# Kernel optimization log

Measured on AMD Instinct MI355X. Metric: run time of the kernel, lower is better.

The kernel has to match this reference:

```python
import jax, jax.numpy as jnp
import numpy as np

D_MODEL = 1024
NUM_TILES = 8
BATCH = 4096
TEMPERATURE = 0.5

gelu = lambda x: jax.nn.gelu(x, approximate=False)  # torch nn.GELU default = exact erf


def setup_inputs() -> dict:
    key = jax.random.key(0)
    ks = jax.random.split(key, 12)
    d, t = D_MODEL, NUM_TILES
    s = lambda fan_in: 1.0 / np.sqrt(fan_in)
    return {
        "x": jax.random.normal(ks[0], (BATCH, d), jnp.float32),
        # router: Linear(d,d) -> GELU -> Linear(d,num_tiles); weights stored (in,out)
        "Wr1": jax.random.uniform(ks[1], (d, d), jnp.float32, -s(d), s(d)),
        "br1": jax.random.uniform(ks[2], (d,), jnp.float32, -s(d), s(d)),
        "Wr2": jax.random.uniform(ks[3], (d, t), jnp.float32, -s(d), s(d)),
        "br2": jax.random.uniform(ks[4], (t,), jnp.float32, -s(d), s(d)),
        # tile nets: Linear(d,2d) -> GELU -> Linear(2d,d), stacked over tiles
        "W1": jax.random.uniform(ks[5], (t, d, 2 * d), jnp.float32, -s(d), s(d)),
        "b1": jax.random.uniform(ks[6], (t, 2 * d), jnp.float32, -s(d), s(d)),
        "W2": jax.random.uniform(ks[7], (t, 2 * d, d), jnp.float32, -s(2 * d), s(2 * d)),
        "b2": jax.random.uniform(ks[8], (t, d), jnp.float32, -s(2 * d), s(2 * d)),
        # output projection Linear(d,d)
        "Wo": jax.random.uniform(ks[9], (d, d), jnp.float32, -s(d), s(d)),
        "bo": jax.random.uniform(ks[10], (d,), jnp.float32, -s(d), s(d)),
    }


def reference(x, Wr1, br1, Wr2, br2, W1, b1, W2, b2, Wo, bo):
    # router logits / temperature
    route_logits = (gelu(x @ Wr1 + br1) @ Wr2 + br2) / TEMPERATURE  # (B, T)
    tile_idx = jnp.argmax(route_logits, axis=-1)                    # (B,)

    # hard routing: compute all tile MLPs, then select the argmax tile per token
    # (dense equivalent of per-sample dispatch; same math as the torch loop)
    h = gelu(jnp.einsum("bd,tdf->btf", x, W1) + b1[None])           # (B, T, 2d)
    tile_out = jnp.einsum("btf,tfd->btd", h, W2) + b2[None]         # (B, T, d)
    selected = jnp.take_along_axis(tile_out, tile_idx[:, None, None], axis=1)[:, 0]  # (B, d)

    output = selected @ Wo + bo                                     # (B, d)
    return output, tile_idx, route_logits
```

## Files before the change

### kernel.cpp

```cpp
#include <hip/hip_runtime.h>
#include <hip/hip_bf16.h>
#include <math.h>
#include <stdint.h>

typedef __bf16 bf16_t;
typedef __bf16 bf16x4 __attribute__((ext_vector_type(4)));
typedef __bf16 bf16x8 __attribute__((ext_vector_type(8)));
typedef float  f32x4  __attribute__((ext_vector_type(4)));

#define BATCH   4096
#define DM      1024
#define DFF     2048
#define NTILES  8
#define MAXXB   40

__device__ __forceinline__ float gelu_exact(float x) {
    return 0.5f * x * (1.0f + erff(x * 0.70710678118654752440f));
}

__device__ __forceinline__ void async_ld16(const bf16_t* g, bf16_t* l) {
    __builtin_amdgcn_global_load_lds(
        (const __attribute__((address_space(1))) void*)g,
        (__attribute__((address_space(3))) void*)l, 16, 0, 0);
}

__device__ __forceinline__ f32x4 mfma16(bf16x8 a, bf16x8 b, f32x4 c) {
    return __builtin_amdgcn_mfma_f32_16x16x32_bf16(a, b, c, 0, 0, 0);
}

template<bool LO>
__device__ void tconv64_body(const float* __restrict__ src, bf16_t* __restrict__ outh,
                             bf16_t* __restrict__ outl, int K, int N, int kt, int nt,
                             float4* t ) {
    const int tid = threadIdx.x;
    const int k0 = kt * 64, n0 = nt * 64;
#pragma unroll
    for (int p = 0; p < 4; ++p) {
        int row = p * 16 + (tid >> 4);
        int c = tid & 15;
        float4 v = *(const float4*)(src + (size_t)(k0 + row) * N + n0 + c * 4);
        t[row * 16 + (c ^ ((row >> 2) & 15))] = v;
    }
    __syncthreads();
    const int n = tid >> 2, b = tid & 3;
    const float* tf = (const float*)t;
    float v[16];
#pragma unroll
    for (int i = 0; i < 16; ++i) {
        int k = 16 * b + i;
        int f4 = k * 16 + ((n >> 2) ^ ((k >> 2) & 15));
        v[i] = tf[f4 * 4 + (n & 3)];
    }
    bf16x8 h0, h1;
#pragma unroll
    for (int i = 0; i < 8; ++i) { h0[i] = (bf16_t)v[i]; h1[i] = (bf16_t)v[8 + i]; }
    size_t oi = (size_t)(n0 + n) * K + k0 + 16 * b;
    *(bf16x8*)(outh + oi) = h0;
    *(bf16x8*)(outh + oi + 8) = h1;
    if constexpr (LO) {
        bf16x8 l0, l1;
#pragma unroll
        for (int i = 0; i < 8; ++i) {
            l0[i] = (bf16_t)(v[i] - (float)h0[i]);
            l1[i] = (bf16_t)(v[8 + i] - (float)h1[i]);
        }
        *(bf16x8*)(outl + oi) = l0;
        *(bf16x8*)(outl + oi + 8) = l1;
    }
}

#define NCVT2 2048
#define NSQ64 256
#define NW1   4096
#define NW2   4096
#define PREP_GRID (NCVT2 + NSQ64 + NSQ64 + NW1 + NW2)

__global__ __launch_bounds__(256) void prep_kernel(
    const float* __restrict__ x, const float* __restrict__ Wr1, const float* __restrict__ Wo,
    const float* __restrict__ W1, const float* __restrict__ W2,
    bf16_t* __restrict__ xh, bf16_t* __restrict__ xl,
    bf16_t* __restrict__ Wr1h, bf16_t* __restrict__ Wr1l, bf16_t* __restrict__ Wot,
    bf16_t* __restrict__ W1t, bf16_t* __restrict__ W2t) {
    __shared__ float4 t[64 * 16];
    int b = blockIdx.x;
    if (b < NCVT2) {
        size_t i = (size_t)b * 256 + threadIdx.x;
        const float4* x4 = (const float4*)x;
        float4 v0 = x4[2 * i], v1 = x4[2 * i + 1];
        float f[8] = {v0.x, v0.y, v0.z, v0.w, v1.x, v1.y, v1.z, v1.w};
        bf16x8 h, l;
#pragma unroll
        for (int j = 0; j < 8; ++j) { h[j] = (bf16_t)f[j]; l[j] = (bf16_t)(f[j] - (float)h[j]); }
        *(bf16x8*)(xh + i * 8) = h;
        *(bf16x8*)(xl + i * 8) = l;
        return;
    }
    b -= NCVT2;
    if (b < NSQ64) { tconv64_body<true >(Wr1, Wr1h, Wr1l, DM, DM, b >> 4, b & 15, t); return; }
    b -= NSQ64;
    if (b < NSQ64) { tconv64_body<false>(Wo, Wot, nullptr, DM, DM, b >> 4, b & 15, t); return; }
    b -= NSQ64;
    if (b < NW1) {
        int mat = b >> 9, r = b & 511;
        size_t off = (size_t)mat * DM * DFF;
        tconv64_body<false>(W1 + off, W1t + off, nullptr, DM, DFF, r >> 5, r & 31, t);
        return;
    }
    b -= NW1;
    {
        int mat = b >> 9, r = b & 511;
        size_t off = (size_t)mat * DM * DFF;
        tconv64_body<false>(W2 + off, W2t + off, nullptr, DFF, DM, r >> 4, r & 15, t);
    }
}

template<bool SPLIT, bool GATHER, bool GELU, bool SCATTER, bool OUTF32>
__global__ __launch_bounds__(512) void gemm_kernel(
    const bf16_t* __restrict__ A, const bf16_t* __restrict__ Alo,
    const bf16_t* __restrict__ Bt, const bf16_t* __restrict__ Btlo,
    const float* __restrict__ bias,
    float* __restrict__ outF, bf16_t* __restrict__ outB,
    const int* __restrict__ perm, const int* __restrict__ counts,
    int M, int N, int K) {
    int tile = 0, rb, cnt = M;
    const int* permT = nullptr;
    if constexpr (GATHER) {
        int xb = blockIdx.x, t = 0, c = 0;
        while (t < NTILES) {
            c = counts[t];
            int nbk = (c + 127) >> 7;
            if (xb < nbk) break;
            xb -= nbk; ++t;
        }
        if (t == NTILES) return;
        tile = t;
        rb = xb * 128;
        cnt = c;
        permT = perm + tile * BATCH;
    } else {
        rb = blockIdx.x * 128;
    }
    Bt   += (size_t)tile * K * N;
    if constexpr (SPLIT) Btlo += (size_t)tile * K * N;
    bias += (size_t)tile * N;

    constexpr int BUF = 128 * 32;
    __shared__ __align__(16) bf16_t As[2 * BUF];
    __shared__ __align__(16) bf16_t Bs[2 * BUF];
    __shared__ __align__(16) bf16_t Asl[SPLIT ? 2 * BUF : 8];
    __shared__ __align__(16) bf16_t Bsl[SPLIT ? 2 * BUF : 8];

    const int lane = threadIdx.x & 63;
    const int wave = threadIdx.x >> 6;
    const int wm = wave & 1, wn = wave >> 1;
    const int nb = blockIdx.y * 128;

    const int srow = lane >> 2;
    const int scol = ((lane & 3) ^ (srow & 3)) * 8;
    const int row = wave * 16 + srow;
    int arow;
    if constexpr (GATHER) {
        int pos = rb + row;
        if (pos > cnt - 1) pos = cnt - 1;
        arow = permT[pos];
    } else {
        arow = rb + row;
    }
    const size_t aoff = (size_t)arow * K + scol;
    const size_t boff = (size_t)(nb + row) * K + scol;

    f32x4 acc[4][2];
#pragma unroll
    for (int i = 0; i < 4; ++i)
#pragma unroll
        for (int j = 0; j < 2; ++j) acc[i][j] = (f32x4){0.f, 0.f, 0.f, 0.f};

    const int lr = lane & 15, lq = lane >> 4;
    const int rdoff = (lr * 4 + (lq ^ (lr & 3))) * 8;

    auto stage = [&](int k0, int buf) {
        async_ld16(A  + aoff + k0, &As[buf * BUF + wave * 512]);
        async_ld16(Bt + boff + k0, &Bs[buf * BUF + wave * 512]);
        if constexpr (SPLIT) {
            async_ld16(Alo  + aoff + k0, &Asl[buf * BUF + wave * 512]);
            async_ld16(Btlo + boff + k0, &Bsl[buf * BUF + wave * 512]);
        }
    };

    auto compute = [&](int cur) {
        bf16x8 af[4], bfr[2], afl[4], bfl[2];
#pragma unroll
        for (int i = 0; i < 4; ++i) {
            af[i] = *(const bf16x8*)&As[cur * BUF + (wm * 4 + i) * 512 + rdoff];
            if constexpr (SPLIT)
                afl[i] = *(const bf16x8*)&Asl[cur * BUF + (wm * 4 + i) * 512 + rdoff];
        }
#pragma unroll
        for (int j = 0; j < 2; ++j) {
            bfr[j] = *(const bf16x8*)&Bs[cur * BUF + (wn * 2 + j) * 512 + rdoff];
            if constexpr (SPLIT)
                bfl[j] = *(const bf16x8*)&Bsl[cur * BUF + (wn * 2 + j) * 512 + rdoff];
        }
#pragma unroll
        for (int i = 0; i < 4; ++i)
#pragma unroll
            for (int j = 0; j < 2; ++j) {
                acc[i][j] = mfma16(af[i], bfr[j], acc[i][j]);
                if constexpr (SPLIT) {
                    acc[i][j] = mfma16(af[i], bfl[j], acc[i][j]);
                    acc[i][j] = mfma16(afl[i], bfr[j], acc[i][j]);
                }
            }
    };

    stage(0, 0);
    int cur = 0;
    for (int k0 = 0; k0 < K; k0 += 32, cur ^= 1) {
        __syncthreads();
        if (k0 + 32 < K) stage(k0 + 32, cur ^ 1);
        compute(cur);
    }

#pragma unroll
    for (int i = 0; i < 4; ++i) {
#pragma unroll
        for (int j = 0; j < 2; ++j) {
#pragma unroll
            for (int r = 0; r < 4; ++r) {
                int m = wm * 64 + i * 16 + lq * 4 + r;
                int n = wn * 32 + j * 16 + lr;
                int pos = rb + m;
                if constexpr (GATHER) { if (pos >= cnt) continue; }
                int grow;
                if constexpr (SCATTER) grow = permT[pos];
                else                   grow = pos;
                int gn = nb + n;
                float v = acc[i][j][r] + bias[gn];
                if constexpr (GELU) v = gelu_exact(v);
                if constexpr (OUTF32) outF[(size_t)grow * N + gn] = v;
                else                  outB[(size_t)grow * N + gn] = (bf16_t)v;
            }
        }
    }
}

__global__ __launch_bounds__(256) void router2_kernel(
    const float* __restrict__ Hr, const float* __restrict__ Wr2, const float* __restrict__ br2,
    float* __restrict__ outLog, float* __restrict__ outIdx,
    int* __restrict__ counts, int* __restrict__ perm) {
    __shared__ float w2s[DM * 9];
    __shared__ int h[NTILES], base[NTILES];
    const int tid = threadIdx.x;
    if (tid < NTILES) h[tid] = 0;
    for (int e = tid; e < DM * 8; e += 256) {
        int k = e >> 3, j = e & 7;
        w2s[k * 9 + j] = Wr2[e];
    }
    __syncthreads();

    const int lane = tid & 63, wave = tid >> 6;
    const int sub = lane >> 4;
    const int lr16 = lane & 15;
    const int row = blockIdx.x * 16 + wave * 4 + sub;

    const float4* Hr4 = (const float4*)Hr;
    float acc[8];
#pragma unroll
    for (int j = 0; j < 8; ++j) acc[j] = 0.f;

#pragma unroll
    for (int i = 0; i < 16; ++i) {
        int f = lr16 + i * 16;
        float4 hv = Hr4[(size_t)row * 256 + f];
        float hx[4] = {hv.x, hv.y, hv.z, hv.w};
        int kbase = f * 4;
#pragma unroll
        for (int d = 0; d < 4; ++d) {
            float xv = hx[d];
            const float* w = &w2s[(kbase + d) * 9];
#pragma unroll
            for (int j = 0; j < 8; ++j) acc[j] += xv * w[j];
        }
    }
#pragma unroll
    for (int off = 8; off; off >>= 1)
#pragma unroll
        for (int j = 0; j < 8; ++j) acc[j] += __shfl_down(acc[j], off);

    int bi = 0, rank = 0;
    if (lr16 == 0) {
        float best = -1e30f;
        float lg[8];
#pragma unroll
        for (int j = 0; j < 8; ++j) {
            float v = (acc[j] + br2[j]) * 2.0f;
            lg[j] = v;
            if (v > best) { best = v; bi = j; }
        }
        float4 lo = {lg[0], lg[1], lg[2], lg[3]};
        float4 hi = {lg[4], lg[5], lg[6], lg[7]};
        *(float4*)(outLog + (size_t)row * 8)     = lo;
        *(float4*)(outLog + (size_t)row * 8 + 4) = hi;
        outIdx[row] = (float)bi;
        rank = atomicAdd(&h[bi], 1);
    }
    __syncthreads();
    if (tid < NTILES && h[tid] > 0) base[tid] = atomicAdd(&counts[tid], h[tid]);
    __syncthreads();
    if (lr16 == 0) perm[bi * BATCH + base[bi] + rank] = row;
}

extern "C" void kernel_launch(void* const* d_in, const int* in_sizes, int n_in,
                              void* d_out, int out_size, void* d_ws, size_t ws_size,
                              hipStream_t stream) {
    const float* x   = (const float*)d_in[0];
    const float* Wr1 = (const float*)d_in[1];
    const float* br1 = (const float*)d_in[2];
    const float* Wr2 = (const float*)d_in[3];
    const float* br2 = (const float*)d_in[4];
    const float* W1  = (const float*)d_in[5];
    const float* b1  = (const float*)d_in[6];
    const float* W2  = (const float*)d_in[7];
    const float* b2  = (const float*)d_in[8];
    const float* Wo  = (const float*)d_in[9];
    const float* bo  = (const float*)d_in[10];

    char* ws = (char*)d_ws;
    size_t o = 0;
    auto carve = [&](size_t bytes) { char* p = ws + o; o = (o + bytes + 255) & ~(size_t)255; return p; };
    bf16_t* Wr1h = (bf16_t*)carve((size_t)DM * DM * 2);
    bf16_t* Wr1l = (bf16_t*)carve((size_t)DM * DM * 2);
    bf16_t* Wot  = (bf16_t*)carve((size_t)DM * DM * 2);
    bf16_t* W1t  = (bf16_t*)carve((size_t)NTILES * DM * DFF * 2);
    bf16_t* W2t  = (bf16_t*)carve((size_t)NTILES * DM * DFF * 2);
    bf16_t* xh   = (bf16_t*)carve((size_t)BATCH * DM * 2);
    bf16_t* xl   = (bf16_t*)carve((size_t)BATCH * DM * 2);
    bf16_t* H1   = (bf16_t*)carve((size_t)BATCH * DFF * 2);
    bf16_t* sel  = (bf16_t*)carve((size_t)BATCH * DM * 2);
    float*  Hr   = (float*)carve((size_t)BATCH * DM * 4);
    int*    counts = (int*)carve(NTILES * sizeof(int));
    int*    perm   = (int*)carve((size_t)NTILES * BATCH * sizeof(int));

    float* outMain = (float*)d_out;
    float* outIdx  = outMain + (size_t)BATCH * DM;
    float* outLog  = outIdx + BATCH;

    hipMemsetAsync(counts, 0, NTILES * sizeof(int), stream);

    prep_kernel<<<PREP_GRID, 256, 0, stream>>>(x, Wr1, Wo, W1, W2,
                                               xh, xl, Wr1h, Wr1l, Wot, W1t, W2t);

    gemm_kernel<true, false, true, false, true><<<dim3(BATCH / 128, DM / 128, 1), 512, 0, stream>>>(
        xh, xl, Wr1h, Wr1l, br1, Hr, nullptr, nullptr, nullptr, BATCH, DM, DM);

    router2_kernel<<<BATCH / 16, 256, 0, stream>>>(Hr, Wr2, br2, outLog, outIdx, counts, perm);

    gemm_kernel<false, true, true, true, false><<<dim3(MAXXB, DFF / 128, 1), 512, 0, stream>>>(
        xh, nullptr, W1t, nullptr, b1, nullptr, H1, perm, counts, BATCH, DFF, DM);

    gemm_kernel<false, true, false, true, false><<<dim3(MAXXB, DM / 128, 1), 512, 0, stream>>>(
        H1, nullptr, W2t, nullptr, b2, nullptr, sel, perm, counts, BATCH, DM, DFF);

    gemm_kernel<false, false, false, false, true><<<dim3(BATCH / 128, DM / 128, 1), 512, 0, stream>>>(
        sel, nullptr, Wot, nullptr, bo, outMain, nullptr, nullptr, nullptr, BATCH, DM, DM);
}
```

Measured before the change: 365.4 us.

## Triple-buffer GEMM LDS pipeline and stream low-precision split operands through registers

Replaces the two-stage LDS double buffer, which synchronised every K step, with a three-stage ring. Explicit vmcnt waits and raw barriers let each tile prefetch two steps ahead. For the split-precision path, the low-part A and B fragments are now loaded straight from global memory into registers one step ahead instead of being staged through LDS. MFMA sections are raised in wave priority with s_setprio. This aims to hide global-load latency and cut LDS traffic and footprint. The risk is that the hand-set vmcnt counts are wrong, and the direct low-part loads ignore the gather permutation on the A rows.

```diff
diff --git a/kernel.cpp b/kernel.cpp
--- a/kernel.cpp
+++ b/kernel.cpp
@@ -145,10 +145,8 @@
     bias += (size_t)tile * N;
 
     constexpr int BUF = 128 * 32;
-    __shared__ __align__(16) bf16_t As[2 * BUF];
-    __shared__ __align__(16) bf16_t Bs[2 * BUF];
-    __shared__ __align__(16) bf16_t Asl[SPLIT ? 2 * BUF : 8];
-    __shared__ __align__(16) bf16_t Bsl[SPLIT ? 2 * BUF : 8];
+    __shared__ __align__(16) bf16_t As[3 * BUF];
+    __shared__ __align__(16) bf16_t Bs[3 * BUF];
 
     const int lane = threadIdx.x & 63;
     const int wave = threadIdx.x >> 6;
@@ -178,47 +176,80 @@
     const int lr = lane & 15, lq = lane >> 4;
     const int rdoff = (lr * 4 + (lq ^ (lr & 3))) * 8;
 
+    size_t aloOff[4], bloOff[2];
+    if constexpr (SPLIT) {
+#pragma unroll
+        for (int i = 0; i < 4; ++i)
+            aloOff[i] = (size_t)(rb + (wm * 4 + i) * 16 + lr) * K + lq * 8;
+#pragma unroll
+        for (int j = 0; j < 2; ++j)
+            bloOff[j] = (size_t)(nb + (wn * 2 + j) * 16 + lr) * K + lq * 8;
+    }
+
     auto stage = [&](int k0, int buf) {
         async_ld16(A  + aoff + k0, &As[buf * BUF + wave * 512]);
         async_ld16(Bt + boff + k0, &Bs[buf * BUF + wave * 512]);
+    };
+
+    auto loadLo = [&](int k0, bf16x8* a, bf16x8* b) {
+#pragma unroll
+        for (int i = 0; i < 4; ++i) a[i] = *(const bf16x8*)(Alo  + aloOff[i] + k0);
+#pragma unroll
+        for (int j = 0; j < 2; ++j) b[j] = *(const bf16x8*)(Btlo + bloOff[j] + k0);
+    };
+
+    auto compute = [&](int cur, const bf16x8* afl, const bf16x8* bfl) {
+        bf16x8 af[4], bfr[2];
+#pragma unroll
+        for (int i = 0; i < 4; ++i)
+            af[i] = *(const bf16x8*)&As[cur * BUF + (wm * 4 + i) * 512 + rdoff];
+#pragma unroll
+        for (int j = 0; j < 2; ++j)
+            bfr[j] = *(const bf16x8*)&Bs[cur * BUF + (wn * 2 + j) * 512 + rdoff];
+        __builtin_amdgcn_s_setprio(1);
+#pragma unroll
+        for (int i = 0; i < 4; ++i)
+#pragma unroll
+            for (int j = 0; j < 2; ++j)
+                acc[i][j] = mfma16(af[i], bfr[j], acc[i][j]);
         if constexpr (SPLIT) {
-            async_ld16(Alo  + aoff + k0, &Asl[buf * BUF + wave * 512]);
-            async_ld16(Btlo + boff + k0, &Bsl[buf * BUF + wave * 512]);
-        }
-    };
-
-    auto compute = [&](int cur) {
-        bf16x8 af[4], bfr[2], afl[4], bfl[2];
-#pragma unroll
-        for (int i = 0; i < 4; ++i) {
-            af[i] = *(const bf16x8*)&As[cur * BUF + (wm * 4 + i) * 512 + rdoff];
-            if constexpr (SPLIT)
-                afl[i] = *(const bf16x8*)&Asl[cur * BUF + (wm * 4 + i) * 512 + rdoff];
-        }
-#pragma unroll
-        for (int j = 0; j < 2; ++j) {
-            bfr[j] = *(const bf16x8*)&Bs[cur * BUF + (wn * 2 + j) * 512 + rdoff];
-            if constexpr (SPLIT)
-                bfl[j] = *(const bf16x8*)&Bsl[cur * BUF + (wn * 2 + j) * 512 + rdoff];
-        }
-#pragma unroll
-        for (int i = 0; i < 4; ++i)
-#pragma unroll
-            for (int j = 0; j < 2; ++j) {
-                acc[i][j] = mfma16(af[i], bfr[j], acc[i][j]);
-                if constexpr (SPLIT) {
+#pragma unroll
+            for (int i = 0; i < 4; ++i)
+#pragma unroll
+                for (int j = 0; j < 2; ++j) {
                     acc[i][j] = mfma16(af[i], bfl[j], acc[i][j]);
                     acc[i][j] = mfma16(afl[i], bfr[j], acc[i][j]);
                 }
-            }
+        }
+        __builtin_amdgcn_s_setprio(0);
     };
 
+    bf16x8 aflC[4], bflC[2], aflN[4], bflN[2];
     stage(0, 0);
-    int cur = 0;
-    for (int k0 = 0; k0 < K; k0 += 32, cur ^= 1) {
-        __syncthreads();
-        if (k0 + 32 < K) stage(k0 + 32, cur ^ 1);
-        compute(cur);
+    stage(32, 1);
+    if constexpr (SPLIT) loadLo(0, aflN, bflN);
+
+    int bufc = 0;
+    for (int k0 = 0; k0 < K; k0 += 32) {
+        if (k0 + 32 < K) {
+            if constexpr (SPLIT) asm volatile("s_waitcnt vmcnt(8)" ::: "memory");
+            else                 asm volatile("s_waitcnt vmcnt(2)" ::: "memory");
+        } else {
+            asm volatile("s_waitcnt vmcnt(0)" ::: "memory");
+        }
+        __builtin_amdgcn_s_barrier();
+        int nb3 = bufc + 2; if (nb3 >= 3) nb3 -= 3;
+        if (k0 + 64 < K) stage(k0 + 64, nb3);
+        if constexpr (SPLIT) {
+#pragma unroll
+            for (int i = 0; i < 4; ++i) aflC[i] = aflN[i];
+#pragma unroll
+            for (int j = 0; j < 2; ++j) bflC[j] = bflN[j];
+            if (k0 + 32 < K) loadLo(k0 + 32, aflN, bflN);
+        }
+        __builtin_amdgcn_sched_barrier(0);
+        compute(bufc, aflC, bflC);
+        if (++bufc == 3) bufc = 0;
     }
 
 #pragma unroll
```

After: 399.2 us. +9.3%, slower.

## Pipeline weight transpose-convert with async LDS loads over four-tile slabs

Applied to the files above, without the earlier changes.

The prep kernel's transpose-and-convert of weights now has each block process a slab of four 64x64 tiles instead of one. It uses global_load_lds async copies into a double-buffered shared tile, so the next tile's load overlaps the current tile's transpose and bf16 store. This cuts the block count and the load latency exposed per tile. In exchange it doubles LDS per block, adds manual waitcnt/barrier sequencing, and leaves fewer blocks to spread across CUs.

```diff
diff --git a/kernel.cpp b/kernel.cpp
--- a/kernel.cpp
+++ b/kernel.cpp
@@ -29,51 +29,79 @@
 }
 
 template<bool LO>
-__device__ void tconv64_body(const float* __restrict__ src, bf16_t* __restrict__ outh,
-                             bf16_t* __restrict__ outl, int K, int N, int kt, int nt,
-                             float4* t ) {
+__device__ void tslab_body(const float* __restrict__ src, bf16_t* __restrict__ outh,
+                           bf16_t* __restrict__ outl, int K, int N, int kt, int nt0,
+                           float4* t ) {
     const int tid = threadIdx.x;
-    const int k0 = kt * 64, n0 = nt * 64;
-#pragma unroll
-    for (int p = 0; p < 4; ++p) {
-        int row = p * 16 + (tid >> 4);
-        int c = tid & 15;
-        float4 v = *(const float4*)(src + (size_t)(k0 + row) * N + n0 + c * 4);
-        t[row * 16 + (c ^ ((row >> 2) & 15))] = v;
-    }
-    __syncthreads();
-    const int n = tid >> 2, b = tid & 3;
-    const float* tf = (const float*)t;
-    float v[16];
-#pragma unroll
-    for (int i = 0; i < 16; ++i) {
-        int k = 16 * b + i;
-        int f4 = k * 16 + ((n >> 2) ^ ((k >> 2) & 15));
-        v[i] = tf[f4 * 4 + (n & 3)];
-    }
-    bf16x8 h0, h1;
-#pragma unroll
-    for (int i = 0; i < 8; ++i) { h0[i] = (bf16_t)v[i]; h1[i] = (bf16_t)v[8 + i]; }
-    size_t oi = (size_t)(n0 + n) * K + k0 + 16 * b;
-    *(bf16x8*)(outh + oi) = h0;
-    *(bf16x8*)(outh + oi + 8) = h1;
-    if constexpr (LO) {
-        bf16x8 l0, l1;
-#pragma unroll
-        for (int i = 0; i < 8; ++i) {
-            l0[i] = (bf16_t)(v[i] - (float)h0[i]);
-            l1[i] = (bf16_t)(v[8 + i] - (float)h1[i]);
-        }
-        *(bf16x8*)(outl + oi) = l0;
-        *(bf16x8*)(outl + oi + 8) = l1;
+    const int lane = tid & 63, wave = tid >> 6;
+    const int k0 = kt * 64;
+    const int lrow4 = lane >> 4;
+    const int slot = lane & 15;
+
+    auto issue = [&](int s, int buf) {
+        const int n0 = (nt0 + s) * 64;
+        float4* base0 = t + buf * 1024;
+#pragma unroll
+        for (int p = 0; p < 4; ++p) {
+            int row = p * 16 + wave * 4 + lrow4;
+            int csrc = slot ^ ((row >> 2) & 15);
+            async_ld16((const bf16_t*)(src + (size_t)(k0 + row) * N + n0 + csrc * 4),
+                       (bf16_t*)(base0 + (p * 16 + wave * 4) * 16));
+        }
+    };
+
+    auto phase2 = [&](int s, int buf) {
+        const int n0 = (nt0 + s) * 64;
+        const float* tf = (const float*)(t + buf * 1024);
+        const int n = tid >> 2, b = tid & 3;
+        float v[16];
+#pragma unroll
+        for (int i = 0; i < 16; ++i) {
+            int k = 16 * b + i;
+            int f4 = k * 16 + ((n >> 2) ^ ((k >> 2) & 15));
+            v[i] = tf[f4 * 4 + (n & 3)];
+        }
+        bf16x8 h0, h1;
+#pragma unroll
+        for (int i = 0; i < 8; ++i) { h0[i] = (bf16_t)v[i]; h1[i] = (bf16_t)v[8 + i]; }
+        size_t oi = (size_t)(n0 + n) * K + k0 + 16 * b;
+        *(bf16x8*)(outh + oi) = h0;
+        *(bf16x8*)(outh + oi + 8) = h1;
+        if constexpr (LO) {
+            bf16x8 l0, l1;
+#pragma unroll
+            for (int i = 0; i < 8; ++i) {
+                l0[i] = (bf16_t)(v[i] - (float)h0[i]);
+                l1[i] = (bf16_t)(v[8 + i] - (float)h1[i]);
+            }
+            *(bf16x8*)(outl + oi) = l0;
+            *(bf16x8*)(outl + oi + 8) = l1;
+        }
+    };
+
+    issue(0, 0);
+#pragma unroll
+    for (int s = 0; s < 4; ++s) {
+        if (s < 3) {
+            issue(s + 1, (s + 1) & 1);
+            asm volatile("s_waitcnt vmcnt(4)" ::: "memory");
+        } else {
+            asm volatile("s_waitcnt vmcnt(0)" ::: "memory");
+        }
+        __builtin_amdgcn_s_barrier();
+        __builtin_amdgcn_sched_barrier(0);
+        phase2(s, s & 1);
+        __builtin_amdgcn_sched_barrier(0);
+        if (s < 3) __builtin_amdgcn_s_barrier();
+        __builtin_amdgcn_sched_barrier(0);
     }
 }
 
 #define NCVT2 2048
-#define NSQ64 256
-#define NW1   4096
-#define NW2   4096
-#define PREP_GRID (NCVT2 + NSQ64 + NSQ64 + NW1 + NW2)
+#define NSLAB_SQ 64
+#define NSLAB_W1 1024
+#define NSLAB_W2 1024
+#define PREP_GRID (NCVT2 + NSLAB_SQ + NSLAB_SQ + NSLAB_W1 + NSLAB_W2)
 
 __global__ __launch_bounds__(256) void prep_kernel(
     const float* __restrict__ x, const float* __restrict__ Wr1, const float* __restrict__ Wo,
@@ -81,7 +109,7 @@
     bf16_t* __restrict__ xh, bf16_t* __restrict__ xl,
     bf16_t* __restrict__ Wr1h, bf16_t* __restrict__ Wr1l, bf16_t* __restrict__ Wot,
     bf16_t* __restrict__ W1t, bf16_t* __restrict__ W2t) {
-    __shared__ float4 t[64 * 16];
+    __shared__ float4 t[2 * 64 * 16];
     int b = blockIdx.x;
     if (b < NCVT2) {
         size_t i = (size_t)b * 256 + threadIdx.x;
@@ -96,21 +124,21 @@
         return;
     }
     b -= NCVT2;
-    if (b < NSQ64) { tconv64_body<true >(Wr1, Wr1h, Wr1l, DM, DM, b >> 4, b & 15, t); return; }
-    b -= NSQ64;
-    if (b < NSQ64) { tconv64_body<false>(Wo, Wot, nullptr, DM, DM, b >> 4, b & 15, t); return; }
-    b -= NSQ64;
-    if (b < NW1) {
-        int mat = b >> 9, r = b & 511;
+    if (b < NSLAB_SQ) { tslab_body<true >(Wr1, Wr1h, Wr1l, DM, DM, b >> 2, (b & 3) * 4, t); return; }
+    b -= NSLAB_SQ;
+    if (b < NSLAB_SQ) { tslab_body<false>(Wo, Wot, nullptr, DM, DM, b >> 2, (b & 3) * 4, t); return; }
+    b -= NSLAB_SQ;
+    if (b < NSLAB_W1) {
+        int mat = b >> 7, r = b & 127;
         size_t off = (size_t)mat * DM * DFF;
-        tconv64_body<false>(W1 + off, W1t + off, nullptr, DM, DFF, r >> 5, r & 31, t);
+        tslab_body<false>(W1 + off, W1t + off, nullptr, DM, DFF, r >> 3, (r & 7) * 4, t);
         return;
     }
-    b -= NW1;
+    b -= NSLAB_W1;
     {
-        int mat = b >> 9, r = b & 511;
+        int mat = b >> 7, r = b & 127;
         size_t off = (size_t)mat * DM * DFF;
-        tconv64_body<false>(W2 + off, W2t + off, nullptr, DFF, DM, r >> 4, r & 15, t);
+        tslab_body<false>(W2 + off, W2t + off, nullptr, DFF, DM, r >> 2, (r & 3) * 4, t);
     }
 }
 
```

Result: no change. 371.0 us (+1.5%).
